# Kernel optimization log

Hardware: AMD Instinct MI355X
Metric: run time of the kernel (lower is better)

## Reference

```python
import jax, jax.numpy as jnp
import numpy as np

N, E = 50000, 800000
DIM, H, D = 256, 16, 8          # dim, num_heads, qk_dim
DH = D * H                      # 128
IN_RPE = 18
SCALE = D ** -0.5               # default qk_scale (None -> 1/sqrt(qk_dim))
EPS = 1e-16                     # torch_geometric softmax denominator eps


def setup_inputs() -> dict:
    key = jax.random.key(0)
    ks = jax.random.split(key, 10)
    x = jax.random.normal(ks[0], (N, DIM), dtype=jnp.float32)
    edge_index = jax.random.randint(ks[1], (2, E), 0, N, dtype=jnp.int64)
    edge_attr = jax.random.normal(ks[2], (E, IN_RPE), dtype=jnp.float32)
    # qkv Linear(dim -> 2*D*H + dim)
    Wqkv = jax.random.normal(ks[3], (DIM, 2 * DH + DIM), dtype=jnp.float32) * DIM ** -0.5
    bqkv = jnp.zeros((2 * DH + DIM,), dtype=jnp.float32)
    # k_rpe / q_rpe Linear(in_rpe_dim -> D*H) (heads_share_rpe=False)
    Wk_rpe = jax.random.normal(ks[4], (IN_RPE, DH), dtype=jnp.float32) * IN_RPE ** -0.5
    bk_rpe = jnp.zeros((DH,), dtype=jnp.float32)
    Wq_rpe = jax.random.normal(ks[5], (IN_RPE, DH), dtype=jnp.float32) * IN_RPE ** -0.5
    bq_rpe = jnp.zeros((DH,), dtype=jnp.float32)
    return {"x": x, "edge_index": edge_index, "edge_attr": edge_attr,
            "Wqkv": Wqkv, "bqkv": bqkv,
            "Wk_rpe": Wk_rpe, "bk_rpe": bk_rpe,
            "Wq_rpe": Wq_rpe, "bq_rpe": bq_rpe}


def _segment_softmax(compat, s, num_nodes):
    # numerically-stable softmax over edges grouped by source node s; compat: (E,H)
    m = jax.ops.segment_max(compat, s, num_segments=num_nodes)   # (N,H)
    ex = jnp.exp(compat - m[s])
    den = jax.ops.segment_sum(ex, s, num_segments=num_nodes)     # (N,H)
    return ex / (den[s] + EPS)


def reference(x, edge_index, edge_attr, Wqkv, bqkv, Wk_rpe, bk_rpe, Wq_rpe, bq_rpe):
    n = x.shape[0]
    e = edge_index.shape[1]
    qkv = x @ Wqkv + bqkv                      # (N, 2*DH + DIM)
    q = qkv[:, :DH].reshape(n, H, D)
    k = qkv[:, DH:2 * DH].reshape(n, H, D)
    v = qkv[:, 2 * DH:].reshape(n, H, DIM // H)
    s, t = edge_index[0], edge_index[1]
    qe = q[s] * SCALE                          # (E,H,D)
    ke = k[t]
    ke = ke + (edge_attr @ Wk_rpe + bk_rpe).reshape(e, H, D)
    qe = qe + (edge_attr @ Wq_rpe + bq_rpe).reshape(e, H, D)
    compat = jnp.einsum('ehd,ehd->eh', qe, ke)  # (E,H)
    attn = _segment_softmax(compat, s, n)       # (E,H)
    msg = (v[t] * attn[..., None]).reshape(e, DIM)  # (E,DIM)
    out = jax.ops.segment_sum(msg, s, num_segments=n)  # (N,DIM)
    return out
```

## Files before the change

### kernel.cpp

```cpp
#include <hip/hip_runtime.h>
#include <math.h>

#define DIMX   256
#define HEADS  16
#define QKD    8
#define DH     128
#define QKVW   512
#define INRPE  18
#define SCALE  0.35355339059327373f

typedef __attribute__((ext_vector_type(8))) short bf16x8;
typedef __attribute__((ext_vector_type(4))) float f32x4;

__device__ __forceinline__ void split1(float v, unsigned short& h, unsigned short& l)
{
    unsigned b  = __float_as_uint(v);
    unsigned hb = (b + 0x7FFFu + ((b >> 16) & 1u)) & 0xFFFF0000u;
    h = (unsigned short)(hb >> 16);
    float r = v - __uint_as_float(hb);
    unsigned rb = __float_as_uint(r);
    l = (unsigned short)((rb + 0x7FFFu + ((rb >> 16) & 1u)) >> 16);
}

__global__ __launch_bounds__(256) void convert_x(
    const float* __restrict__ x, unsigned short* __restrict__ xh,
    unsigned short* __restrict__ xl, int Nn, int Mpad)
{
    size_t total = (size_t)Mpad * 64;
    for (size_t i = (size_t)blockIdx.x * blockDim.x + threadIdx.x; i < total;
         i += (size_t)gridDim.x * blockDim.x) {
        size_t row = i >> 6;
        float4 v = make_float4(0.f, 0.f, 0.f, 0.f);
        if (row < (size_t)Nn) v = *(const float4*)&x[i * 4];
        ushort4 h, l;
        split1(v.x, h.x, l.x);
        split1(v.y, h.y, l.y);
        split1(v.z, h.z, l.z);
        split1(v.w, h.w, l.w);
        *(ushort4*)&xh[i * 4] = h;
        *(ushort4*)&xl[i * 4] = l;
    }
}

__global__ __launch_bounds__(256) void convert_w(
    const float* __restrict__ W, unsigned short* __restrict__ wth,
    unsigned short* __restrict__ wtl)
{
    int n = blockIdx.x;
    int k = threadIdx.x;
    float v = W[(size_t)k * QKVW + n];
    unsigned short h, l;
    split1(v, h, l);
    wth[(size_t)n * DIMX + k] = h;
    wtl[(size_t)n * DIMX + k] = l;
}

__global__ __launch_bounds__(256, 2) void qkv_gemm_mfma(
    const unsigned short* __restrict__ xh, const unsigned short* __restrict__ xl,
    const unsigned short* __restrict__ wth, const unsigned short* __restrict__ wtl,
    const float* __restrict__ bias, float* __restrict__ qkv, int Nn)
{
    int tid  = threadIdx.x;
    int w    = tid >> 6, lane = tid & 63;
    int wm   = w >> 1,   wn   = w & 1;
    int row0 = blockIdx.x * 128 + wm * 64;
    int col0 = blockIdx.y * 128 + wn * 64;
    int lrow = lane & 15;
    int lk8  = (lane >> 4) * 8;

    const unsigned short* pah = xh  + (size_t)(row0 + lrow) * DIMX + lk8;
    const unsigned short* pal = xl  + (size_t)(row0 + lrow) * DIMX + lk8;
    const unsigned short* pbh = wth + (size_t)(col0 + lrow) * DIMX + lk8;
    const unsigned short* pbl = wtl + (size_t)(col0 + lrow) * DIMX + lk8;

    f32x4 acc[4][4];
    #pragma unroll
    for (int i = 0; i < 4; i++)
        #pragma unroll
        for (int j = 0; j < 4; j++)
            acc[i][j] = (f32x4){0.f, 0.f, 0.f, 0.f};

    for (int t = 0; t < DIMX / 32; ++t) {
        int kb = t * 32;
        bf16x8 ah[4], al[4], bh[4], bl[4];
        #pragma unroll
        for (int f = 0; f < 4; ++f) {
            ah[f] = *(const bf16x8*)(pah + (size_t)f * 4096 + kb);
            al[f] = *(const bf16x8*)(pal + (size_t)f * 4096 + kb);
            bh[f] = *(const bf16x8*)(pbh + (size_t)f * 4096 + kb);
            bl[f] = *(const bf16x8*)(pbl + (size_t)f * 4096 + kb);
        }
        #pragma unroll
        for (int fm = 0; fm < 4; ++fm)
            #pragma unroll
            for (int fn = 0; fn < 4; ++fn) {
                acc[fm][fn] = __builtin_amdgcn_mfma_f32_16x16x32_bf16(
                    ah[fm], bh[fn], acc[fm][fn], 0, 0, 0);
                acc[fm][fn] = __builtin_amdgcn_mfma_f32_16x16x32_bf16(
                    ah[fm], bl[fn], acc[fm][fn], 0, 0, 0);
                acc[fm][fn] = __builtin_amdgcn_mfma_f32_16x16x32_bf16(
                    al[fm], bh[fn], acc[fm][fn], 0, 0, 0);
            }
    }

    float sc = (blockIdx.y == 0) ? SCALE : 1.0f;
    int rbase = (lane >> 4) * 4;
    #pragma unroll
    for (int fn = 0; fn < 4; ++fn) {
        float bv = bias[col0 + fn * 16 + lrow];
        #pragma unroll
        for (int fm = 0; fm < 4; ++fm) {
            #pragma unroll
            for (int j = 0; j < 4; ++j) {
                int r = row0 + fm * 16 + rbase + j;
                if (r < Nn)
                    qkv[(size_t)r * QKVW + col0 + fn * 16 + lrow] =
                        (acc[fm][fn][j] + bv) * sc;
            }
        }
    }
}

__global__ __launch_bounds__(256) void qkv_gemm(
    const float* __restrict__ x, const float* __restrict__ W,
    const float* __restrict__ bias, float* __restrict__ qkv, int Nn)
{
    __shared__ float As[16][132];
    __shared__ float Bs[16][132];

    int tid  = threadIdx.x;
    int row0 = blockIdx.x * 128;
    int col0 = blockIdx.y * 128;
    int tx = tid & 15, ty = tid >> 4;

    float acc[8][8] = {};

    for (int k0 = 0; k0 < DIMX; k0 += 16) {
        #pragma unroll
        for (int r = 0; r < 2; r++) {
            int idx  = tid + r * 256;
            int arow = idx >> 2, acol = (idx & 3) * 4;
            float4 av = make_float4(0.f, 0.f, 0.f, 0.f);
            int grow = row0 + arow;
            if (grow < Nn) av = *(const float4*)&x[(size_t)grow * DIMX + k0 + acol];
            As[acol + 0][arow] = av.x;
            As[acol + 1][arow] = av.y;
            As[acol + 2][arow] = av.z;
            As[acol + 3][arow] = av.w;
        }
        #pragma unroll
        for (int r = 0; r < 2; r++) {
            int idx  = tid + r * 256;
            int brow = idx >> 5, bcol = (idx & 31) * 4;
            float4 bv = *(const float4*)&W[(size_t)(k0 + brow) * QKVW + col0 + bcol];
            *(float4*)&Bs[brow][bcol] = bv;
        }
        __syncthreads();
        #pragma unroll
        for (int kk = 0; kk < 16; kk++) {
            float a0[8], b0[8];
            *(float4*)&a0[0] = *(const float4*)&As[kk][ty * 8];
            *(float4*)&a0[4] = *(const float4*)&As[kk][ty * 8 + 4];
            *(float4*)&b0[0] = *(const float4*)&Bs[kk][tx * 4];
            *(float4*)&b0[4] = *(const float4*)&Bs[kk][64 + tx * 4];
            #pragma unroll
            for (int i = 0; i < 8; i++)
                #pragma unroll
                for (int j = 0; j < 8; j++)
                    acc[i][j] = fmaf(a0[i], b0[j], acc[i][j]);
        }
        __syncthreads();
    }

    float4 bv0 = *(const float4*)&bias[col0 + tx * 4];
    float4 bv1 = *(const float4*)&bias[col0 + 64 + tx * 4];
    float sc = (col0 == 0) ? SCALE : 1.0f;
    #pragma unroll
    for (int i = 0; i < 8; i++) {
        int grow = row0 + ty * 8 + i;
        if (grow < Nn) {
            float4 o0, o1;
            o0.x = (acc[i][0] + bv0.x) * sc;
            o0.y = (acc[i][1] + bv0.y) * sc;
            o0.z = (acc[i][2] + bv0.z) * sc;
            o0.w = (acc[i][3] + bv0.w) * sc;
            o1.x = (acc[i][4] + bv1.x) * sc;
            o1.y = (acc[i][5] + bv1.y) * sc;
            o1.z = (acc[i][6] + bv1.z) * sc;
            o1.w = (acc[i][7] + bv1.w) * sc;
            *(float4*)&qkv[(size_t)grow * QKVW + col0 + tx * 4] = o0;
            *(float4*)&qkv[(size_t)grow * QKVW + col0 + 64 + tx * 4] = o1;
        }
    }
}

__global__ void count_kernel(const int* __restrict__ ei, int* __restrict__ deg, int E)
{
    int e = blockIdx.x * blockDim.x + threadIdx.x;
    if (e < E) atomicAdd(&deg[ei[e]], 1);
}

__global__ __launch_bounds__(1024) void scan_kernel(
    const int* __restrict__ deg, int* __restrict__ off, int n)
{
    __shared__ int wsum[16];
    __shared__ int wbase[16];
    __shared__ int tot;
    int tid = threadIdx.x;
    int lane = tid & 63, w = tid >> 6;
    int carry = 0;
    for (int base = 0; base < n; base += 1024) {
        int idx = base + tid;
        int v = (idx < n) ? deg[idx] : 0;
        int acc = v;
        #pragma unroll
        for (int d = 1; d < 64; d <<= 1) {
            int u = __shfl_up(acc, d, 64);
            if (lane >= d) acc += u;
        }
        if (lane == 63) wsum[w] = acc;
        __syncthreads();
        if (tid < 16) {
            int s = wsum[tid];
            int a = s;
            #pragma unroll
            for (int d = 1; d < 16; d <<= 1) {
                int u = __shfl_up(a, d, 64);
                if (tid >= d) a += u;
            }
            wbase[tid] = a - s;
            if (tid == 15) tot = a;
        }
        __syncthreads();
        if (idx < n) off[idx] = carry + wbase[w] + (acc - v);
        carry += tot;
        __syncthreads();
    }
    if (tid == 0) off[n] = carry;
}

__global__ void scatter_kernel(const int* __restrict__ ei,
                               const int* __restrict__ off, int* __restrict__ cur,
                               int2* __restrict__ elist, int E)
{
    int e = blockIdx.x * blockDim.x + threadIdx.x;
    if (e < E) {
        int s = ei[e];
        int t = ei[E + e];
        int pos = atomicAdd(&cur[s], 1);
        elist[off[s] + pos] = make_int2(e, t);
    }
}

__global__ __launch_bounds__(128, 2) void node_attn(
    const float* __restrict__ qkv, const int2* __restrict__ elist,
    const int* __restrict__ off, const float* __restrict__ edge_attr,
    const float* __restrict__ Wq_rpe, const float* __restrict__ bq_rpe,
    const float* __restrict__ Wk_rpe, const float* __restrict__ bk_rpe,
    float* __restrict__ out, int Nn)
{
    int tid = threadIdx.x;
    int n = blockIdx.x;
    if (n >= Nn) return;

    float wq[INRPE], wk[INRPE];
    #pragma unroll
    for (int j = 0; j < INRPE; j++) {
        wq[j] = Wq_rpe[j * DH + tid];
        wk[j] = Wk_rpe[j * DH + tid];
    }
    #pragma unroll
    for (int j = 0; j < INRPE; j++) {
        asm volatile("" : "+v"(wq[j]), "+v"(wk[j]));
    }

    float qs = qkv[(size_t)n * QKVW + tid] + bq_rpe[tid];
    float bk = bk_rpe[tid];

    int beg = off[n], end = off[n + 1];

    if (beg == end) {
        *(float2*)&out[(size_t)n * DIMX + 2 * tid] = make_float2(0.f, 0.f);
        return;
    }

    float lsum = 0.0f;
    float2 o = make_float2(0.f, 0.f);

    int2 etc = elist[beg];
    float  ktc = qkv[(size_t)etc.y * QKVW + DH + tid];
    float2 vtc = *(const float2*)&qkv[(size_t)etc.y * QKVW + 2 * DH + 2 * tid];
    float eac[INRPE];
    {
        const float2* p = (const float2*)(edge_attr + (size_t)etc.x * INRPE);
        #pragma unroll
        for (int j = 0; j < 9; j++) { float2 v2 = p[j]; eac[2*j] = v2.x; eac[2*j+1] = v2.y; }
    }
    int2 etn = elist[(beg + 1 < end) ? beg + 1 : beg];

    #pragma unroll 1
    for (int i = beg; i < end; i++) {
        int inx2 = (i + 2 < end) ? i + 2 : end - 1;
        int2 et2 = elist[inx2];
        float  ktn = qkv[(size_t)etn.y * QKVW + DH + tid];
        float2 vtn = *(const float2*)&qkv[(size_t)etn.y * QKVW + 2 * DH + 2 * tid];
        float ean[INRPE];
        {
            const float2* p = (const float2*)(edge_attr + (size_t)etn.x * INRPE);
            #pragma unroll
            for (int j = 0; j < 9; j++) { float2 v2 = p[j]; ean[2*j] = v2.x; ean[2*j+1] = v2.y; }
        }

        float qr = 0.f, kr = bk;
        #pragma unroll
        for (int j = 0; j < INRPE; j++) {
            qr = fmaf(eac[j], wq[j], qr);
            kr = fmaf(eac[j], wk[j], kr);
        }

        float c2 = (qs + qr) * (ktc + kr);
        c2 += __shfl_xor(c2, 1, 64);
        c2 += __shfl_xor(c2, 2, 64);
        c2 += __shfl_xor(c2, 4, 64);

        float ex = __expf(c2);
        lsum += ex;
        o.x = fmaf(ex, vtc.x, o.x);
        o.y = fmaf(ex, vtc.y, o.y);

        etc = etn; etn = et2;
        ktc = ktn; vtc = vtn;
        #pragma unroll
        for (int j = 0; j < INRPE; j++) eac[j] = ean[j];
    }

    float inv = 1.0f / (lsum + 1e-16f);
    *(float2*)&out[(size_t)n * DIMX + 2 * tid] = make_float2(o.x * inv, o.y * inv);
}

extern "C" void kernel_launch(void* const* d_in, const int* in_sizes, int n_in,
                              void* d_out, int out_size, void* d_ws, size_t ws_size,
                              hipStream_t stream)
{
    const float* x    = (const float*)d_in[0];
    const int*   ei   = (const int*)d_in[1];
    const float* ea   = (const float*)d_in[2];
    const float* Wqkv = (const float*)d_in[3];
    const float* bqkv = (const float*)d_in[4];
    const float* Wk   = (const float*)d_in[5];
    const float* bk   = (const float*)d_in[6];
    const float* Wq   = (const float*)d_in[7];
    const float* bq   = (const float*)d_in[8];

    int Nn = in_sizes[0] / DIMX;
    int E  = in_sizes[1] / 2;
    float* out = (float*)d_out;

    int Mblocks = (Nn + 127) / 128;
    int Mpad    = Mblocks * 128;

    size_t qkv_bytes  = (size_t)Nn * QKVW * sizeof(float);
    float* qkv = (float*)d_ws;
    char*  P   = (char*)d_ws + qkv_bytes;

    size_t xpart  = (size_t)Mpad * DIMX * sizeof(unsigned short);
    size_t wpart  = (size_t)QKVW * DIMX * sizeof(unsigned short);
    size_t gemm_bytes = 2 * xpart + 2 * wpart;
    size_t csr_bytes  = sizeof(int) * (size_t)(3 * Nn + 2) + sizeof(int2) * (size_t)E;
    size_t need = qkv_bytes + (gemm_bytes > csr_bytes ? gemm_bytes : csr_bytes);

    int*  deg = (int*)P;
    int*  cur = deg + Nn;
    int*  off = cur + Nn;
    int2* elist = (int2*)(off + ((Nn + 2) & ~1));

    if (ws_size >= need) {
        unsigned short* xh  = (unsigned short*)P;
        unsigned short* xl  = xh + (size_t)Mpad * DIMX;
        unsigned short* wth = xl + (size_t)Mpad * DIMX;
        unsigned short* wtl = wth + (size_t)QKVW * DIMX;

        convert_x<<<2048, 256, 0, stream>>>(x, xh, xl, Nn, Mpad);
        convert_w<<<QKVW, 256, 0, stream>>>(Wqkv, wth, wtl);
        qkv_gemm_mfma<<<dim3(Mblocks, 4), 256, 0, stream>>>(xh, xl, wth, wtl,
                                                            bqkv, qkv, Nn);
    } else {
        qkv_gemm<<<dim3(Mblocks, QKVW / 128), 256, 0, stream>>>(x, Wqkv, bqkv, qkv, Nn);
    }

    hipMemsetAsync(deg, 0, sizeof(int) * 2 * (size_t)Nn, stream);
    count_kernel<<<(E + 255) / 256, 256, 0, stream>>>(ei, deg, E);
    scan_kernel<<<1, 1024, 0, stream>>>(deg, off, Nn);
    scatter_kernel<<<(E + 255) / 256, 256, 0, stream>>>(ei, off, cur, elist, E);
    node_attn<<<Nn, 128, 0, stream>>>(qkv, elist, off, ea, Wq, bq, Wk, bk, out, Nn);
}
```

Measured before the change: 613.8 us.

## Parallelize degree scan and make node attention a persistent grid-stride kernel

```diff
diff --git a/kernel.cpp b/kernel.cpp
--- a/kernel.cpp
+++ b/kernel.cpp
@@ -200,43 +200,80 @@
     if (e < E) atomicAdd(&deg[ei[e]], 1);
 }
 
-__global__ __launch_bounds__(1024) void scan_kernel(
-    const int* __restrict__ deg, int* __restrict__ off, int n)
-{
-    __shared__ int wsum[16];
-    __shared__ int wbase[16];
-    __shared__ int tot;
-    int tid = threadIdx.x;
-    int lane = tid & 63, w = tid >> 6;
+__device__ __forceinline__ int4 load_deg4(const int* __restrict__ deg, int base, int n)
+{
+    int4 v = make_int4(0, 0, 0, 0);
+    if (base + 3 < n) v = *(const int4*)&deg[base];
+    else {
+        if (base + 0 < n) v.x = deg[base + 0];
+        if (base + 1 < n) v.y = deg[base + 1];
+        if (base + 2 < n) v.z = deg[base + 2];
+        if (base + 3 < n) v.w = deg[base + 3];
+    }
+    return v;
+}
+
+__global__ __launch_bounds__(256) void scan_sums(
+    const int* __restrict__ deg, int* __restrict__ psum, int n)
+{
+    int base = blockIdx.x * 1024 + threadIdx.x * 4;
+    int4 v = load_deg4(deg, base, n);
+    int s = v.x + v.y + v.z + v.w;
+    #pragma unroll
+    for (int d = 1; d < 64; d <<= 1) s += __shfl_xor(s, d, 64);
+    __shared__ int ws[4];
+    int lane = threadIdx.x & 63, w = threadIdx.x >> 6;
+    if (lane == 0) ws[w] = s;
+    __syncthreads();
+    if (threadIdx.x == 0) psum[blockIdx.x] = ws[0] + ws[1] + ws[2] + ws[3];
+}
+
+__global__ __launch_bounds__(64) void scan_base(
+    const int* __restrict__ psum, int* __restrict__ pbase,
+    int* __restrict__ off, int n, int nchunk)
+{
+    int t = threadIdx.x;
     int carry = 0;
-    for (int base = 0; base < n; base += 1024) {
-        int idx = base + tid;
-        int v = (idx < n) ? deg[idx] : 0;
-        int acc = v;
+    for (int base = 0; base < nchunk; base += 64) {
+        int v = (base + t < nchunk) ? psum[base + t] : 0;
+        int incl = v;
         #pragma unroll
         for (int d = 1; d < 64; d <<= 1) {
-            int u = __shfl_up(acc, d, 64);
-            if (lane >= d) acc += u;
-        }
-        if (lane == 63) wsum[w] = acc;
-        __syncthreads();
-        if (tid < 16) {
-            int s = wsum[tid];
-            int a = s;
-            #pragma unroll
-            for (int d = 1; d < 16; d <<= 1) {
-                int u = __shfl_up(a, d, 64);
-                if (tid >= d) a += u;
-            }
-            wbase[tid] = a - s;
-            if (tid == 15) tot = a;
-        }
-        __syncthreads();
-        if (idx < n) off[idx] = carry + wbase[w] + (acc - v);
-        carry += tot;
-        __syncthreads();
-    }
-    if (tid == 0) off[n] = carry;
+            int u = __shfl_up(incl, d, 64);
+            if (t >= d) incl += u;
+        }
+        if (base + t < nchunk) pbase[base + t] = carry + incl - v;
+        carry += __shfl(incl, 63, 64);
+    }
+    if (t == 0) off[n] = carry;
+}
+
+__global__ __launch_bounds__(256) void scan_final(
+    const int* __restrict__ deg, const int* __restrict__ pbase,
+    int* __restrict__ off, int n)
+{
+    int base = blockIdx.x * 1024 + threadIdx.x * 4;
+    int4 v = load_deg4(deg, base, n);
+    int e1 = v.x, e2 = e1 + v.y, e3 = e2 + v.z, T = e3 + v.w;
+    int lane = threadIdx.x & 63, w = threadIdx.x >> 6;
+    int incl = T;
+    #pragma unroll
+    for (int d = 1; d < 64; d <<= 1) {
+        int u = __shfl_up(incl, d, 64);
+        if (lane >= d) incl += u;
+    }
+    int lexcl = incl - T;
+    __shared__ int ws[4];
+    if (lane == 63) ws[w] = incl;
+    __syncthreads();
+    int wexcl = 0;
+    #pragma unroll
+    for (int j = 0; j < 4; j++) if (j < w) wexcl += ws[j];
+    int o0 = pbase[blockIdx.x] + wexcl + lexcl;
+    if (base + 0 < n) off[base + 0] = o0;
+    if (base + 1 < n) off[base + 1] = o0 + e1;
+    if (base + 2 < n) off[base + 2] = o0 + e2;
+    if (base + 3 < n) off[base + 3] = o0 + e3;
 }
 
 __global__ void scatter_kernel(const int* __restrict__ ei,
@@ -260,8 +297,6 @@
     float* __restrict__ out, int Nn)
 {
     int tid = threadIdx.x;
-    int n = blockIdx.x;
-    if (n >= Nn) return;
 
     float wq[INRPE], wk[INRPE];
     #pragma unroll
@@ -273,69 +308,93 @@
     for (int j = 0; j < INRPE; j++) {
         asm volatile("" : "+v"(wq[j]), "+v"(wk[j]));
     }
-
-    float qs = qkv[(size_t)n * QKVW + tid] + bq_rpe[tid];
-    float bk = bk_rpe[tid];
-
-    int beg = off[n], end = off[n + 1];
-
-    if (beg == end) {
-        *(float2*)&out[(size_t)n * DIMX + 2 * tid] = make_float2(0.f, 0.f);
-        return;
-    }
-
-    float lsum = 0.0f;
-    float2 o = make_float2(0.f, 0.f);
-
-    int2 etc = elist[beg];
-    float  ktc = qkv[(size_t)etc.y * QKVW + DH + tid];
-    float2 vtc = *(const float2*)&qkv[(size_t)etc.y * QKVW + 2 * DH + 2 * tid];
-    float eac[INRPE];
-    {
-        const float2* p = (const float2*)(edge_attr + (size_t)etc.x * INRPE);
-        #pragma unroll
-        for (int j = 0; j < 9; j++) { float2 v2 = p[j]; eac[2*j] = v2.x; eac[2*j+1] = v2.y; }
-    }
-    int2 etn = elist[(beg + 1 < end) ? beg + 1 : beg];
-
-    #pragma unroll 1
-    for (int i = beg; i < end; i++) {
-        int inx2 = (i + 2 < end) ? i + 2 : end - 1;
-        int2 et2 = elist[inx2];
-        float  ktn = qkv[(size_t)etn.y * QKVW + DH + tid];
-        float2 vtn = *(const float2*)&qkv[(size_t)etn.y * QKVW + 2 * DH + 2 * tid];
-        float ean[INRPE];
+    float bqv = bq_rpe[tid];
+    float bkv = bk_rpe[tid];
+
+    for (int n = blockIdx.x; n < Nn; n += gridDim.x) {
+        int beg = off[n], end = off[n + 1];
+        if (beg == end) {
+            *(float2*)&out[(size_t)n * DIMX + 2 * tid] = make_float2(0.f, 0.f);
+            continue;
+        }
+        float qs = qkv[(size_t)n * QKVW + tid] + bqv;
+
+        float lsum = 0.0f;
+        float2 o = make_float2(0.f, 0.f);
+
+        int2 etA = elist[beg];
+        int eA = __builtin_amdgcn_readfirstlane(etA.x);
+        float  ktA = qkv[(size_t)etA.y * QKVW + DH + tid];
+        float2 vtA = *(const float2*)&qkv[(size_t)etA.y * QKVW + 2 * DH + 2 * tid];
+        float eaA[INRPE];
         {
-            const float2* p = (const float2*)(edge_attr + (size_t)etn.x * INRPE);
+            const float2* p = (const float2*)(edge_attr + (size_t)eA * INRPE);
             #pragma unroll
-            for (int j = 0; j < 9; j++) { float2 v2 = p[j]; ean[2*j] = v2.x; ean[2*j+1] = v2.y; }
-        }
-
-        float qr = 0.f, kr = bk;
-        #pragma unroll
-        for (int j = 0; j < INRPE; j++) {
-            qr = fmaf(eac[j], wq[j], qr);
-            kr = fmaf(eac[j], wk[j], kr);
-        }
-
-        float c2 = (qs + qr) * (ktc + kr);
-        c2 += __shfl_xor(c2, 1, 64);
-        c2 += __shfl_xor(c2, 2, 64);
-        c2 += __shfl_xor(c2, 4, 64);
-
-        float ex = __expf(c2);
-        lsum += ex;
-        o.x = fmaf(ex, vtc.x, o.x);
-        o.y = fmaf(ex, vtc.y, o.y);
-
-        etc = etn; etn = et2;
-        ktc = ktn; vtc = vtn;
-        #pragma unroll
-        for (int j = 0; j < INRPE; j++) eac[j] = ean[j];
-    }
-
-    float inv = 1.0f / (lsum + 1e-16f);
-    *(float2*)&out[(size_t)n * DIMX + 2 * tid] = make_float2(o.x * inv, o.y * inv);
+            for (int j = 0; j < 9; j++) { float2 u = p[j]; eaA[2*j] = u.x; eaA[2*j+1] = u.y; }
+        }
+
+        for (int i = beg; i < end; i += 2) {
+            bool hasB = (i + 1 < end);
+            float ktB = 0.f; float2 vtB = make_float2(0.f, 0.f);
+            float eaB[INRPE];
+            if (hasB) {
+                int2 etB = elist[i + 1];
+                int eB = __builtin_amdgcn_readfirstlane(etB.x);
+                ktB = qkv[(size_t)etB.y * QKVW + DH + tid];
+                vtB = *(const float2*)&qkv[(size_t)etB.y * QKVW + 2 * DH + 2 * tid];
+                const float2* p = (const float2*)(edge_attr + (size_t)eB * INRPE);
+                #pragma unroll
+                for (int j = 0; j < 9; j++) { float2 u = p[j]; eaB[2*j] = u.x; eaB[2*j+1] = u.y; }
+            }
+
+            {
+                float qr = 0.f, kr = bkv;
+                #pragma unroll
+                for (int j = 0; j < INRPE; j++) {
+                    qr = fmaf(eaA[j], wq[j], qr);
+                    kr = fmaf(eaA[j], wk[j], kr);
+                }
+                float c2 = (qs + qr) * (ktA + kr);
+                c2 += __shfl_xor(c2, 1, 64);
+                c2 += __shfl_xor(c2, 2, 64);
+                c2 += __shfl_xor(c2, 4, 64);
+                float ex = __expf(c2);
+                lsum += ex;
+                o.x = fmaf(ex, vtA.x, o.x);
+                o.y = fmaf(ex, vtA.y, o.y);
+            }
+
+            if (i + 2 < end) {
+                int2 et2 = elist[i + 2];
+                int eN = __builtin_amdgcn_readfirstlane(et2.x);
+                ktA = qkv[(size_t)et2.y * QKVW + DH + tid];
+                vtA = *(const float2*)&qkv[(size_t)et2.y * QKVW + 2 * DH + 2 * tid];
+                const float2* p = (const float2*)(edge_attr + (size_t)eN * INRPE);
+                #pragma unroll
+                for (int j = 0; j < 9; j++) { float2 u = p[j]; eaA[2*j] = u.x; eaA[2*j+1] = u.y; }
+            }
+
+            if (hasB) {
+                float qr = 0.f, kr = bkv;
+                #pragma unroll
+                for (int j = 0; j < INRPE; j++) {
+                    qr = fmaf(eaB[j], wq[j], qr);
+                    kr = fmaf(eaB[j], wk[j], kr);
+                }
+                float c2 = (qs + qr) * (ktB + kr);
+                c2 += __shfl_xor(c2, 1, 64);
+                c2 += __shfl_xor(c2, 2, 64);
+                c2 += __shfl_xor(c2, 4, 64);
+                float ex = __expf(c2);
+                lsum += ex;
+                o.x = fmaf(ex, vtB.x, o.x);
+                o.y = fmaf(ex, vtB.y, o.y);
+            }
+        }
+
+        float inv = 1.0f / (lsum + 1e-16f);
+        *(float2*)&out[(size_t)n * DIMX + 2 * tid] = make_float2(o.x * inv, o.y * inv);
+    }
 }
 
 extern "C" void kernel_launch(void* const* d_in, const int* in_sizes, int n_in,
@@ -358,6 +417,7 @@
 
     int Mblocks = (Nn + 127) / 128;
     int Mpad    = Mblocks * 128;
+    int nchunk  = (Nn + 1023) / 1024;
 
     size_t qkv_bytes  = (size_t)Nn * QKVW * sizeof(float);
     float* qkv = (float*)d_ws;
@@ -366,13 +426,16 @@
     size_t xpart  = (size_t)Mpad * DIMX * sizeof(unsigned short);
     size_t wpart  = (size_t)QKVW * DIMX * sizeof(unsigned short);
     size_t gemm_bytes = 2 * xpart + 2 * wpart;
-    size_t csr_bytes  = sizeof(int) * (size_t)(3 * Nn + 2) + sizeof(int2) * (size_t)E;
+    size_t csr_bytes  = sizeof(int) * (size_t)(3 * Nn + 2 + 2 * nchunk + 8)
+                      + sizeof(int2) * (size_t)E;
     size_t need = qkv_bytes + (gemm_bytes > csr_bytes ? gemm_bytes : csr_bytes);
 
     int*  deg = (int*)P;
     int*  cur = deg + Nn;
     int*  off = cur + Nn;
     int2* elist = (int2*)(off + ((Nn + 2) & ~1));
+    int*  psum  = (int*)(elist + E);
+    int*  pbase = psum + nchunk;
 
     if (ws_size >= need) {
         unsigned short* xh  = (unsigned short*)P;
@@ -390,7 +453,11 @@
 
     hipMemsetAsync(deg, 0, sizeof(int) * 2 * (size_t)Nn, stream);
     count_kernel<<<(E + 255) / 256, 256, 0, stream>>>(ei, deg, E);
-    scan_kernel<<<1, 1024, 0, stream>>>(deg, off, Nn);
+    scan_sums<<<nchunk, 256, 0, stream>>>(deg, psum, Nn);
+    scan_base<<<1, 64, 0, stream>>>(psum, pbase, off, Nn, nchunk);
+    scan_final<<<nchunk, 256, 0, stream>>>(deg, pbase, off, Nn);
     scatter_kernel<<<(E + 255) / 256, 256, 0, stream>>>(ei, off, cur, elist, E);
-    node_attn<<<Nn, 128, 0, stream>>>(qkv, elist, off, ea, Wq, bq, Wk, bk, out, Nn);
-}
+
+    int nb = 4096 < Nn ? 4096 : Nn;
+    node_attn<<<nb, 128, 0, stream>>>(qkv, elist, off, ea, Wq, bq, Wk, bk, out, Nn);
+}
```

After: 656.3 us. 6.9% more time.
